# Performance work log

Measured on AMD Instinct MI355X. Metric: run time of the kernel, lower is better.

## Reference

```python
import jax, jax.numpy as jnp
import numpy as np

B, C, L = 8, 512, 4096
CK, CV = C // 8, C // 2  # 64, 256


def maxpool2(t):
    # max_pool1d(kernel=2, stride=2) over last axis: [B, c, L] -> [B, c, L//2]
    b, c, l = t.shape
    return t.reshape(b, c, l // 2, 2).max(axis=-1)


def setup_inputs() -> dict:
    key = jax.random.key(0)
    ks = jax.random.split(key, 6)
    return {
        "x": jax.random.normal(ks[0], (B, C, L), dtype=jnp.float32),
        "W_theta": jax.random.normal(ks[1], (CK, C), dtype=jnp.float32) * 0.02,
        "W_phi": jax.random.normal(ks[2], (CK, C), dtype=jnp.float32) * 0.02,
        "W_g": jax.random.normal(ks[3], (CV, C), dtype=jnp.float32) * 0.02,
        "W_o": jax.random.normal(ks[4], (C, CV), dtype=jnp.float32) * 0.02,
        "gamma": jax.random.normal(ks[5], (), dtype=jnp.float32),
    }


def reference(x, W_theta, W_phi, W_g, W_o, gamma):
    # 1x1 convs are channel matmuls
    theta = jnp.einsum("kc,bcl->bkl", W_theta, x)            # [B, C/8, L]
    phi = maxpool2(jnp.einsum("kc,bcl->bkl", W_phi, x))      # [B, C/8, L/2]
    g = maxpool2(jnp.einsum("vc,bcl->bvl", W_g, x))          # [B, C/2, L/2]
    # attention scores over downsampled keys: [B, L, L/2]
    scores = jnp.einsum("bkl,bkm->blm", theta, phi)
    beta = jax.nn.softmax(scores, axis=-1)
    # aggregate values: g @ beta^T -> [B, C/2, L]
    o_in = jnp.einsum("bvm,blm->bvl", g, beta)
    o = jnp.einsum("ov,bvl->bol", W_o, o_in)                 # [B, C, L]
    return gamma * o + x
```

## Files before the change

### kernel.cpp

```cpp
#include <hip/hip_runtime.h>
#include <cstdint>
#include <cstddef>

#define B_ 8
#define C_ 512
#define L_ 4096
#define M_ 2048
#define CK_ 64
#define CV_ 256

typedef _Float16 f16;
typedef _Float16 f16x8 __attribute__((ext_vector_type(8)));
typedef _Float16 f16x4 __attribute__((ext_vector_type(4)));
typedef float f32x4 __attribute__((ext_vector_type(4)));
typedef float f32x16 __attribute__((ext_vector_type(16)));
typedef unsigned int u32x4 __attribute__((ext_vector_type(4)));

#define MFMA16(A, Bv, Cv) __builtin_amdgcn_mfma_f32_16x16x32_f16(A, Bv, Cv, 0, 0, 0)
#define MFMA32(A, Bv, Cv) __builtin_amdgcn_mfma_f32_32x32x16_f16(A, Bv, Cv, 0, 0, 0)

#define LOG2E 1.44269504f

static __device__ __forceinline__ uint32_t pkrtz(float a, float b) {
    return __builtin_bit_cast(uint32_t, __builtin_amdgcn_cvt_pkrtz(a, b));
}

__global__ __launch_bounds__(256) void cvt_all(const float* __restrict__ Wt,
                                               const float* __restrict__ Wp,
                                               const float* __restrict__ Wg,
                                               const float* __restrict__ Wo,
                                               f16* __restrict__ WallF,
                                               f16* __restrict__ WoF) {
    const int i = blockIdx.x * 256 + threadIdx.x;
    const int NW = 384 * 512;
    if (i < NW) {
        const int och = i >> 9, c = i & 511;
        float v;
        if (och < 64)       v = Wt[i];
        else if (och < 128) v = Wp[i - 64 * 512];
        else                v = Wg[i - 128 * 512];
        const int idx = (((och >> 4) * 16 + (c >> 5)) * 64 +
                         (((c >> 3) & 3) << 4) + (och & 15)) * 8 + (c & 7);
        WallF[idx] = (f16)v;
    } else {
        const int j = i - NW;
        const int oc = j >> 8, v = j & 255;
        const int idx = (((oc >> 4) * 8 + (v >> 5)) * 64 +
                         (((v >> 3) & 3) << 4) + (oc & 15)) * 8 + (v & 7);
        WoF[idx] = (f16)Wo[j];
    }
}

__global__ __launch_bounds__(256) void fused_proj(const f16* __restrict__ WallF,
                                                  const float* __restrict__ x,
                                                  f16* __restrict__ theta2,
                                                  f16* __restrict__ phi2,
                                                  f16* __restrict__ g2) {
    __shared__ __align__(16) f16 xs[64][32][8];
    const int b    = blockIdx.y;
    const int l0   = blockIdx.x * 32;
    const int tid  = threadIdx.x;
    const int w    = tid >> 6;
    const int lane = tid & 63;
    const int lq   = lane & 15;
    const int g    = lane >> 4;
    const int wb   = w * 96;

    {
        const float* xb = x + (size_t)b * C_ * L_ + l0 + (tid & 31);
        const int co0 = tid >> 5;
#pragma unroll
        for (int i = 0; i < 8; ++i) {
            const int co = i * 8 + co0;
            float v[8];
#pragma unroll
            for (int j = 0; j < 8; ++j) v[j] = xb[(size_t)(co * 8 + j) * L_];
            u32x4 p = {pkrtz(v[0], v[1]), pkrtz(v[2], v[3]),
                       pkrtz(v[4], v[5]), pkrtz(v[6], v[7])};
            *reinterpret_cast<u32x4*>(&xs[co][tid & 31][0]) = p;
        }
    }
    __syncthreads();

    f32x4 acc[6][2] = {};
    for (int ks = 0; ks < 16; ++ks) {
        f16x8 Bf[2];
#pragma unroll
        for (int lt = 0; lt < 2; ++lt)
            Bf[lt] = *reinterpret_cast<const f16x8*>(&xs[ks * 4 + g][lt * 16 + lq][0]);
#pragma unroll
        for (int t = 0; t < 6; ++t) {
            f16x8 Af = *reinterpret_cast<const f16x8*>(
                WallF + (((size_t)(6 * w + t) * 16 + ks) * 64 + lane) * 8);
            acc[t][0] = MFMA16(Af, Bf[0], acc[t][0]);
            acc[t][1] = MFMA16(Af, Bf[1], acc[t][1]);
        }
    }

#pragma unroll
    for (int t = 0; t < 6; ++t) {
        const int och0 = wb + t * 16;
#pragma unroll
        for (int lt = 0; lt < 2; ++lt) {
            const int l = l0 + lt * 16 + lq;
            if (och0 < 64) {
#pragma unroll
                for (int r = 0; r < 4; ++r) {
                    const int och = och0 + 4 * g + r;
                    theta2[(((size_t)b * 8 + (och >> 3)) * L_ + l) * 8 + (och & 7)] =
                        (f16)(acc[t][lt][r] * LOG2E);
                }
            } else {
#pragma unroll
                for (int r = 0; r < 4; ++r) {
                    const float pv = fmaxf(acc[t][lt][r], __shfl_xor(acc[t][lt][r], 1));
                    if (!(lane & 1)) {
                        const int m = l >> 1;
                        if (och0 < 128) {
                            const int kc = och0 - 64 + 4 * g + r;
                            phi2[(((size_t)b * 8 + (kc >> 3)) * M_ + m) * 8 + (kc & 7)] =
                                (f16)pv;
                        } else {
                            const int vc = och0 - 128 + 4 * g + r;
                            g2[(((size_t)b * 256 + (m >> 3)) * CV_ + vc) * 8 + (m & 7)] =
                                (f16)pv;
                        }
                    }
                }
            }
        }
    }
}

__global__ __launch_bounds__(512, 4) void attn_flash(const f16* __restrict__ theta2,
                                                     const f16* __restrict__ phi2,
                                                     const f16* __restrict__ g2,
                                                     f16* __restrict__ op,
                                                     float* __restrict__ mlm,
                                                     float* __restrict__ mll) {
    const int bid = blockIdx.x;
    const int mh  = blockIdx.y;
    const int b   = bid & 7;
    const int qt  = bid >> 3;
    const int w   = threadIdx.x >> 6;
    const int qg  = w >> 2;
    const int vq  = w & 3;
    const int q0  = qt * 64 + qg * 32;
    const int vb  = vq * 64;
    const int lane = threadIdx.x & 63;
    const int lq   = lane & 31;
    const int hi   = lane >> 5;

    const f16* qbase = theta2 + (size_t)b * 8 * L_ * 8;
    f16x8 Qf[4];
#pragma unroll
    for (int f = 0; f < 4; ++f)
        Qf[f] = *reinterpret_cast<const f16x8*>(
            qbase + ((size_t)(2 * f + hi) * L_ + q0 + lq) * 8);

    f32x16 acc[2] = {};
    float m_run = -3.0e38f;
    float l_run = 0.f;

    const f16* kbase = phi2 + (size_t)b * 8 * M_ * 8;
    const f16* vbase = g2 + (size_t)b * 256 * CV_ * 8;

    uint32_t ko[4], vo[4];
#pragma unroll
    for (int f = 0; f < 4; ++f) ko[f] = ((2 * f + hi) * M_ + mh * 1024 + lq) * 8u;
#pragma unroll
    for (int ch = 0; ch < 2; ++ch)
#pragma unroll
        for (int vt = 0; vt < 2; ++vt)
            vo[ch * 2 + vt] = ((mh * 128 + 2 * ch + hi) * CV_ + vb + vt * 32 + lq) * 8u;

    for (int it = 0; it < 32; ++it) {
        f16x8 Kf[4];
#pragma unroll
        for (int f = 0; f < 4; ++f)
            Kf[f] = *reinterpret_cast<const f16x8*>(kbase + ko[f]);
        f16x8 Vf[2][2];
#pragma unroll
        for (int ch = 0; ch < 2; ++ch)
#pragma unroll
            for (int vt = 0; vt < 2; ++vt)
                Vf[ch][vt] = *reinterpret_cast<const f16x8*>(vbase + vo[ch * 2 + vt]);

        f32x16 S = {};
        __builtin_amdgcn_s_setprio(1);
#pragma unroll
        for (int f = 0; f < 4; ++f) S = MFMA32(Kf[f], Qf[f], S);
        __builtin_amdgcn_s_setprio(0);

        float t0 = fmaxf(fmaxf(S[0], S[1]), S[2]);
        float t1 = fmaxf(fmaxf(S[3], S[4]), S[5]);
        float t2 = fmaxf(fmaxf(S[6], S[7]), S[8]);
        float t3 = fmaxf(fmaxf(S[9], S[10]), S[11]);
        float t4 = fmaxf(fmaxf(S[12], S[13]), S[14]);
        float tm = fmaxf(fmaxf(fmaxf(t0, t1), t2),
                         fmaxf(fmaxf(t3, t4), S[15]));
        tm = fmaxf(tm, __shfl_xor(tm, 32));
        if (__any(tm > m_run + 11.5f)) {
            const float m_new = fmaxf(m_run, tm);
            const float sc = __builtin_amdgcn_exp2f(m_run - m_new);
#pragma unroll
            for (int vt = 0; vt < 2; ++vt)
#pragma unroll
                for (int r = 0; r < 16; ++r) acc[vt][r] *= sc;
            l_run *= sc;
            m_run = m_new;
        }
        float s[16];
#pragma unroll
        for (int r = 0; r < 16; ++r) s[r] = __builtin_amdgcn_exp2f(S[r] - m_run);
        float a0 = (s[0] + s[1]) + (s[2] + s[3]);
        float a1 = (s[4] + s[5]) + (s[6] + s[7]);
        float a2 = (s[8] + s[9]) + (s[10] + s[11]);
        float a3 = (s[12] + s[13]) + (s[14] + s[15]);
        l_run += (a0 + a1) + (a2 + a3);

        uint32_t pk[8];
#pragma unroll
        for (int i = 0; i < 8; ++i) pk[i] = pkrtz(s[2 * i], s[2 * i + 1]);
        asm volatile("v_permlane32_swap_b32 %0, %1" : "+v"(pk[0]), "+v"(pk[2]));
        asm volatile("v_permlane32_swap_b32 %0, %1" : "+v"(pk[1]), "+v"(pk[3]));
        asm volatile("v_permlane32_swap_b32 %0, %1" : "+v"(pk[4]), "+v"(pk[6]));
        asm volatile("v_permlane32_swap_b32 %0, %1" : "+v"(pk[5]), "+v"(pk[7]));
        u32x4 fr0 = {pk[0], pk[1], pk[2], pk[3]};
        u32x4 fr1 = {pk[4], pk[5], pk[6], pk[7]};
        f16x8 P0 = __builtin_bit_cast(f16x8, fr0);
        f16x8 P1 = __builtin_bit_cast(f16x8, fr1);

        __builtin_amdgcn_s_setprio(1);
#pragma unroll
        for (int vt = 0; vt < 2; ++vt) acc[vt] = MFMA32(Vf[0][vt], P0, acc[vt]);
#pragma unroll
        for (int vt = 0; vt < 2; ++vt) acc[vt] = MFMA32(Vf[1][vt], P1, acc[vt]);
        __builtin_amdgcn_s_setprio(0);

#pragma unroll
        for (int f = 0; f < 4; ++f) ko[f] += 32u * 8u;
#pragma unroll
        for (int i = 0; i < 4; ++i) vo[i] += 4u * CV_ * 8u;
    }

    const float l_full = l_run + __shfl_xor(l_run, 32);
    const float inv = 1.f / l_full;
    const int qtile = (q0 >> 4) + (lq >> 4);
    const int ql    = lq & 15;
    f16* opm = op + (size_t)mh * B_ * L_ * CV_;
#pragma unroll
    for (int vt = 0; vt < 2; ++vt)
#pragma unroll
        for (int rq = 0; rq < 4; ++rq) {
            f16x4 o;
#pragma unroll
            for (int j = 0; j < 4; ++j) o[j] = (f16)(acc[vt][4 * rq + j] * inv);
            f16* p = opm + ((((size_t)b * 256 + qtile) * 8 + vq * 2 + vt) * 64 +
                            rq * 16 + ql) * 8 + 4 * hi;
            *reinterpret_cast<f16x4*>(p) = o;
        }
    if (vq == 0 && hi == 0) {
        const int q = q0 + lq;
        mlm[(size_t)mh * B_ * L_ + (size_t)b * L_ + q] = m_run;
        mll[(size_t)mh * B_ * L_ + (size_t)b * L_ + q] = l_full;
    }
}

__global__ __launch_bounds__(256) void combine(const f16* __restrict__ opA,
                                               const f16* __restrict__ opB,
                                               const float* __restrict__ mlm,
                                               const float* __restrict__ mll,
                                               f16* __restrict__ o2) {
    const int c = blockIdx.x * 256 + threadIdx.x;
    const int lane  = c & 63;
    const int qtile = (c >> 9) & 255;
    const int b     = c >> 17;
    const int q     = qtile * 16 + (lane & 15);
    const size_t mi = (size_t)b * L_ + q;
    const float mA = mlm[mi],            lA = mll[mi];
    const float mB = mlm[B_ * L_ + mi],  lB = mll[B_ * L_ + mi];
    const float ms = fmaxf(mA, mB);
    const float wA = __builtin_amdgcn_exp2f(mA - ms) * lA;
    const float wB = __builtin_amdgcn_exp2f(mB - ms) * lB;
    const float d  = wA + wB;
    const float aA = wA / d, aB = wB / d;
    const f16x8 va = *reinterpret_cast<const f16x8*>(opA + (size_t)c * 8);
    const f16x8 vb = *reinterpret_cast<const f16x8*>(opB + (size_t)c * 8);
    f16x8 o;
#pragma unroll
    for (int j = 0; j < 8; ++j)
        o[j] = (f16)((float)va[j] * aA + (float)vb[j] * aB);
    *reinterpret_cast<f16x8*>(o2 + (size_t)c * 8) = o;
}

__global__ __launch_bounds__(256) void out_mfma(const f16* __restrict__ WoF,
                                                const f16* __restrict__ o2,
                                                const float* __restrict__ x,
                                                const float* __restrict__ gamma_p,
                                                float* __restrict__ out) {
    const int b    = blockIdx.z;
    const int l0   = blockIdx.x * 64;
    const int wid  = threadIdx.x >> 6;
    const int oc0  = blockIdx.y * 64 + wid * 16;
    const int lane = threadIdx.x & 63;
    const int lq   = lane & 15;
    const int g    = lane >> 4;

    f32x4 acc[4] = {{0.f, 0.f, 0.f, 0.f}, {0.f, 0.f, 0.f, 0.f},
                    {0.f, 0.f, 0.f, 0.f}, {0.f, 0.f, 0.f, 0.f}};
#pragma unroll
    for (int ks = 0; ks < 8; ++ks) {
        f16x8 A = *reinterpret_cast<const f16x8*>(
            WoF + (((size_t)(oc0 >> 4) * 8 + ks) * 64 + lane) * 8);
#pragma unroll
        for (int lt = 0; lt < 4; ++lt) {
            const f16* bp = o2 + (((size_t)(b * 256 + (l0 >> 4) + lt) * 8 + ks) * 64 +
                                  lane) * 8;
            acc[lt] = MFMA16(A, *reinterpret_cast<const f16x8*>(bp), acc[lt]);
        }
    }
    const float gamma = *gamma_p;
#pragma unroll
    for (int lt = 0; lt < 4; ++lt)
#pragma unroll
        for (int r = 0; r < 4; ++r) {
            const size_t o = ((size_t)b * C_ + oc0 + 4 * g + r) * L_ + l0 + lt * 16 + lq;
            out[o] = fmaf(gamma, acc[lt][r], x[o]);
        }
}

extern "C" void kernel_launch(void* const* d_in, const int* in_sizes, int n_in,
                              void* d_out, int out_size, void* d_ws, size_t ws_size,
                              hipStream_t stream) {
    const float* x       = (const float*)d_in[0];
    const float* W_theta = (const float*)d_in[1];
    const float* W_phi   = (const float*)d_in[2];
    const float* W_g     = (const float*)d_in[3];
    const float* W_o     = (const float*)d_in[4];
    const float* gamma   = (const float*)d_in[5];
    float* out = (float*)d_out;

    f16* theta2 = (f16*)d_ws;
    f16* phi2   = theta2 + (size_t)B_ * 8 * L_ * 8;
    f16* g2     = phi2 + (size_t)B_ * 8 * M_ * 8;
    f16* op     = g2 + (size_t)B_ * 256 * CV_ * 8;
    f16* o2     = op;
    f16* WoF    = op + (size_t)2 * B_ * L_ * CV_;
    f16* WallF  = WoF + (size_t)C_ * CV_;
    float* mlm  = (float*)(WallF + (size_t)384 * C_);
    float* mll  = mlm + (size_t)2 * B_ * L_;

    const int cvt_n = 384 * 512 + 512 * 256;
    cvt_all<<<dim3(cvt_n / 256), 256, 0, stream>>>(W_theta, W_phi, W_g, W_o, WallF, WoF);
    fused_proj<<<dim3(L_ / 32, B_), 256, 0, stream>>>(WallF, x, theta2, phi2, g2);
    attn_flash<<<dim3(512, 2), 512, 0, stream>>>(theta2, phi2, g2, op, mlm, mll);
    combine<<<dim3((B_ * L_ * CV_ / 8) / 256), 256, 0, stream>>>(
        op, op + (size_t)B_ * L_ * CV_, mlm, mll, o2);
    out_mfma<<<dim3(L_ / 64, C_ / 64, B_), 256, 0, stream>>>(WoF, o2, x, gamma, out);
}
```

Baseline: 187.0 us.

## Widen per-wave value tile in flash attention to halve redundant QK work

```diff
diff --git a/kernel.cpp b/kernel.cpp
--- a/kernel.cpp
+++ b/kernel.cpp
@@ -132,7 +132,7 @@
     }
 }
 
-__global__ __launch_bounds__(512, 4) void attn_flash(const f16* __restrict__ theta2,
+__global__ __launch_bounds__(256, 3) void attn_flash(const f16* __restrict__ theta2,
                                                      const f16* __restrict__ phi2,
                                                      const f16* __restrict__ g2,
                                                      f16* __restrict__ op,
@@ -143,10 +143,10 @@
     const int b   = bid & 7;
     const int qt  = bid >> 3;
     const int w   = threadIdx.x >> 6;
-    const int qg  = w >> 2;
-    const int vq  = w & 3;
+    const int qg  = w >> 1;
+    const int vq  = w & 1;
     const int q0  = qt * 64 + qg * 32;
-    const int vb  = vq * 64;
+    const int vb  = vq * 128;
     const int lane = threadIdx.x & 63;
     const int lq   = lane & 31;
     const int hi   = lane >> 5;
@@ -158,33 +158,25 @@
         Qf[f] = *reinterpret_cast<const f16x8*>(
             qbase + ((size_t)(2 * f + hi) * L_ + q0 + lq) * 8);
 
-    f32x16 acc[2] = {};
+    f32x16 acc[4] = {};
     float m_run = -3.0e38f;
     float l_run = 0.f;
 
     const f16* kbase = phi2 + (size_t)b * 8 * M_ * 8;
     const f16* vbase = g2 + (size_t)b * 256 * CV_ * 8;
 
-    uint32_t ko[4], vo[4];
+    uint32_t ko[4], vo[2];
 #pragma unroll
     for (int f = 0; f < 4; ++f) ko[f] = ((2 * f + hi) * M_ + mh * 1024 + lq) * 8u;
 #pragma unroll
     for (int ch = 0; ch < 2; ++ch)
-#pragma unroll
-        for (int vt = 0; vt < 2; ++vt)
-            vo[ch * 2 + vt] = ((mh * 128 + 2 * ch + hi) * CV_ + vb + vt * 32 + lq) * 8u;
+        vo[ch] = ((mh * 128 + 2 * ch + hi) * CV_ + vb + lq) * 8u;
 
     for (int it = 0; it < 32; ++it) {
         f16x8 Kf[4];
 #pragma unroll
         for (int f = 0; f < 4; ++f)
             Kf[f] = *reinterpret_cast<const f16x8*>(kbase + ko[f]);
-        f16x8 Vf[2][2];
-#pragma unroll
-        for (int ch = 0; ch < 2; ++ch)
-#pragma unroll
-            for (int vt = 0; vt < 2; ++vt)
-                Vf[ch][vt] = *reinterpret_cast<const f16x8*>(vbase + vo[ch * 2 + vt]);
 
         f32x16 S = {};
         __builtin_amdgcn_s_setprio(1);
@@ -204,24 +196,23 @@
             const float m_new = fmaxf(m_run, tm);
             const float sc = __builtin_amdgcn_exp2f(m_run - m_new);
 #pragma unroll
-            for (int vt = 0; vt < 2; ++vt)
+            for (int vt = 0; vt < 4; ++vt)
 #pragma unroll
                 for (int r = 0; r < 16; ++r) acc[vt][r] *= sc;
             l_run *= sc;
             m_run = m_new;
         }
-        float s[16];
-#pragma unroll
-        for (int r = 0; r < 16; ++r) s[r] = __builtin_amdgcn_exp2f(S[r] - m_run);
-        float a0 = (s[0] + s[1]) + (s[2] + s[3]);
-        float a1 = (s[4] + s[5]) + (s[6] + s[7]);
-        float a2 = (s[8] + s[9]) + (s[10] + s[11]);
-        float a3 = (s[12] + s[13]) + (s[14] + s[15]);
+#pragma unroll
+        for (int r = 0; r < 16; ++r) S[r] = __builtin_amdgcn_exp2f(S[r] - m_run);
+        float a0 = (S[0] + S[1]) + (S[2] + S[3]);
+        float a1 = (S[4] + S[5]) + (S[6] + S[7]);
+        float a2 = (S[8] + S[9]) + (S[10] + S[11]);
+        float a3 = (S[12] + S[13]) + (S[14] + S[15]);
         l_run += (a0 + a1) + (a2 + a3);
 
         uint32_t pk[8];
 #pragma unroll
-        for (int i = 0; i < 8; ++i) pk[i] = pkrtz(s[2 * i], s[2 * i + 1]);
+        for (int i = 0; i < 8; ++i) pk[i] = pkrtz(S[2 * i], S[2 * i + 1]);
         asm volatile("v_permlane32_swap_b32 %0, %1" : "+v"(pk[0]), "+v"(pk[2]));
         asm volatile("v_permlane32_swap_b32 %0, %1" : "+v"(pk[1]), "+v"(pk[3]));
         asm volatile("v_permlane32_swap_b32 %0, %1" : "+v"(pk[4]), "+v"(pk[6]));
@@ -231,17 +222,31 @@
         f16x8 P0 = __builtin_bit_cast(f16x8, fr0);
         f16x8 P1 = __builtin_bit_cast(f16x8, fr1);
 
-        __builtin_amdgcn_s_setprio(1);
-#pragma unroll
-        for (int vt = 0; vt < 2; ++vt) acc[vt] = MFMA32(Vf[0][vt], P0, acc[vt]);
-#pragma unroll
-        for (int vt = 0; vt < 2; ++vt) acc[vt] = MFMA32(Vf[1][vt], P1, acc[vt]);
-        __builtin_amdgcn_s_setprio(0);
+        {
+            f16x8 Vf0[4];
+#pragma unroll
+            for (int vt = 0; vt < 4; ++vt)
+                Vf0[vt] = *reinterpret_cast<const f16x8*>(vbase + vo[0] + vt * 32 * 8);
+            __builtin_amdgcn_s_setprio(1);
+#pragma unroll
+            for (int vt = 0; vt < 4; ++vt) acc[vt] = MFMA32(Vf0[vt], P0, acc[vt]);
+            __builtin_amdgcn_s_setprio(0);
+        }
+        {
+            f16x8 Vf1[4];
+#pragma unroll
+            for (int vt = 0; vt < 4; ++vt)
+                Vf1[vt] = *reinterpret_cast<const f16x8*>(vbase + vo[1] + vt * 32 * 8);
+            __builtin_amdgcn_s_setprio(1);
+#pragma unroll
+            for (int vt = 0; vt < 4; ++vt) acc[vt] = MFMA32(Vf1[vt], P1, acc[vt]);
+            __builtin_amdgcn_s_setprio(0);
+        }
 
 #pragma unroll
         for (int f = 0; f < 4; ++f) ko[f] += 32u * 8u;
-#pragma unroll
-        for (int i = 0; i < 4; ++i) vo[i] += 4u * CV_ * 8u;
+        vo[0] += 4u * CV_ * 8u;
+        vo[1] += 4u * CV_ * 8u;
     }
 
     const float l_full = l_run + __shfl_xor(l_run, 32);
@@ -250,13 +255,13 @@
     const int ql    = lq & 15;
     f16* opm = op + (size_t)mh * B_ * L_ * CV_;
 #pragma unroll
-    for (int vt = 0; vt < 2; ++vt)
+    for (int vt = 0; vt < 4; ++vt)
 #pragma unroll
         for (int rq = 0; rq < 4; ++rq) {
             f16x4 o;
 #pragma unroll
             for (int j = 0; j < 4; ++j) o[j] = (f16)(acc[vt][4 * rq + j] * inv);
-            f16* p = opm + ((((size_t)b * 256 + qtile) * 8 + vq * 2 + vt) * 64 +
+            f16* p = opm + ((((size_t)b * 256 + qtile) * 8 + vq * 4 + vt) * 64 +
                             rq * 16 + ql) * 8 + 4 * hi;
             *reinterpret_cast<f16x4*>(p) = o;
         }
@@ -354,7 +359,7 @@
     const int cvt_n = 384 * 512 + 512 * 256;
     cvt_all<<<dim3(cvt_n / 256), 256, 0, stream>>>(W_theta, W_phi, W_g, W_o, WallF, WoF);
     fused_proj<<<dim3(L_ / 32, B_), 256, 0, stream>>>(WallF, x, theta2, phi2, g2);
-    attn_flash<<<dim3(512, 2), 512, 0, stream>>>(theta2, phi2, g2, op, mlm, mll);
+    attn_flash<<<dim3(512, 2), 256, 0, stream>>>(theta2, phi2, g2, op, mlm, mll);
     combine<<<dim3((B_ * L_ * CV_ / 8) / 256), 256, 0, stream>>>(
         op, op + (size_t)B_ * L_ * CV_, mlm, mll, o2);
     out_mfma<<<dim3(L_ / 64, C_ / 64, B_), 256, 0, stream>>>(WoF, o2, x, gamma, out);
```

After: 157.7 us. 1.19x faster.
